# Performance work log

Hardware: AMD Instinct MI355X
Metric: run time of the kernel (lower is better)

## Reference

```python
import jax, jax.numpy as jnp
import numpy as np

NEG = jnp.float32(-1e10)

def setup_inputs() -> dict:
    key = jax.random.key(0)
    k1, k2, k3, k4 = jax.random.split(key, 4)
    B, Ns, Nr, D = 64, 512, 256, 1024
    return {
        "span_embeddings": jax.random.normal(k1, (B, Ns, D), dtype=jnp.float32),
        "image_embeddings": jax.random.normal(k2, (B, Nr, D), dtype=jnp.float32),
        "span_mask": jax.random.randint(k3, (B, Ns), 0, 2).astype(jnp.int32),
        "image_mask": jax.random.randint(k4, (B, Nr), 0, 2).astype(jnp.int32),
    }

def reference(span_embeddings, image_embeddings, span_mask, image_mask):
    # pair mask: (B, Ns, Nr) = image_mask[b, None, r] * span_mask[b, s, None]
    mask = (image_mask[:, None, :] * span_mask[:, :, None]).astype(span_embeddings.dtype)
    # QK^T with multiplicative mask, then custom zero->-1e10 masking
    att = jnp.einsum('bsd,brd->bsr', span_embeddings, image_embeddings) * mask
    att = jnp.where(att != 0, att, NEG)
    # spans attend over ROIs
    w_first = jax.nn.softmax(att, axis=-1) * mask
    att_first = jnp.einsum('bsr,brd->bsd', w_first, image_embeddings)
    score = jnp.mean(jnp.square(span_embeddings - att_first))
    # ROIs attend over spans (score_type='both')
    att_t = jnp.swapaxes(att, 1, 2)            # (B, Nr, Ns)
    w_second = jax.nn.softmax(att_t, axis=-1) * jnp.swapaxes(mask, 1, 2)
    att_second = jnp.einsum('brs,bsd->brd', w_second, span_embeddings)
    score = score + jnp.mean(jnp.square(image_embeddings - att_second))
    return score, att_first, att
```

## Files before the change

### kernel.cpp

```cpp
#include <hip/hip_runtime.h>
#include <hip/hip_bf16.h>
#include <math.h>

#define B_  64
#define NS  512
#define NR  256
#define DD  1024
#define NEGV (-1e10f)

typedef __attribute__((ext_vector_type(4))) float f32x4;
typedef __attribute__((ext_vector_type(8))) short bf16x8;

__device__ __forceinline__ unsigned short f2bf(float x) {
    unsigned u = __builtin_bit_cast(unsigned, x);
    unsigned r = u + 0x7FFFu + ((u >> 16) & 1u);
    return (unsigned short)(r >> 16);
}
__device__ __forceinline__ unsigned pk2(float x, float y) {
    unsigned r;
    asm("v_cvt_pk_bf16_f32 %0, %1, %2" : "=v"(r) : "v"(x), "v"(y));
    return r;
}
__device__ __forceinline__ void pk_hilo(float x, float y, unsigned& h, unsigned& l) {
    h = pk2(x, y);
    const float hx = __builtin_bit_cast(float, h << 16);
    const float hy = __builtin_bit_cast(float, h & 0xFFFF0000u);
    l = pk2(x - hx, y - hy);
}
__device__ __forceinline__ void gload16(const void* g, void* l) {
    __builtin_amdgcn_global_load_lds((const __attribute__((address_space(1))) void*)g,
                                     (__attribute__((address_space(3))) void*)l, 16, 0, 0);
}

__global__ __launch_bounds__(64) void zero_ws(double* ws) {
    if (threadIdx.x == 0) { ws[0] = 0.0; ws[1] = 0.0; }
}

__global__ __launch_bounds__(256) void att_mfma(
    const float* __restrict__ span, const float* __restrict__ image,
    const int* __restrict__ smask, const int* __restrict__ imask,
    float* __restrict__ att, float2* __restrict__ rowP, float2* __restrict__ colP,
    int doStats) {
    const int b  = blockIdx.z;
    const int s0 = blockIdx.y * 128;
    const int r0 = blockIdx.x * 128;
    __shared__ unsigned short Ah[128][40], Al[128][40], Bh[128][40], Bl[128][40];
    __shared__ float2 rowLDS[128][2];
    __shared__ float2 colLDS[128][2];
    const int tid  = threadIdx.x;
    const int lane = tid & 63;
    const int w    = tid >> 6;
    const int wso  = (w >> 1) * 64;
    const int wro  = (w & 1) * 64;
    const float* Sp = span  + ((size_t)b * NS + s0) * DD;
    const float* Im = image + ((size_t)b * NR + r0) * DD;

    f32x4 acc[4][4];
    #pragma unroll
    for (int i = 0; i < 4; ++i)
        #pragma unroll
        for (int j = 0; j < 4; ++j) acc[i][j] = (f32x4){0.f, 0.f, 0.f, 0.f};

    const int krel = (tid & 7) * 4;
    const int row0 = tid >> 3;
    const int fr   = lane & 15;
    const int fk   = (lane >> 4) * 8;

    float4 pa[4], pc[4];
    auto LOADK = [&](int k0) {
        #pragma unroll
        for (int p = 0; p < 4; ++p) {
            const int row = row0 + p * 32;
            pa[p] = *reinterpret_cast<const float4*>(Sp + (size_t)row * DD + k0 + krel);
            pc[p] = *reinterpret_cast<const float4*>(Im + (size_t)row * DD + k0 + krel);
        }
    };
    auto CONVW = [&]() {
        #pragma unroll
        for (int p = 0; p < 4; ++p) {
            const int row = row0 + p * 32;
            unsigned h0, l0, h1, l1;
            uint2 u;
            pk_hilo(pa[p].x, pa[p].y, h0, l0); pk_hilo(pa[p].z, pa[p].w, h1, l1);
            u.x = h0; u.y = h1; *reinterpret_cast<uint2*>(&Ah[row][krel]) = u;
            u.x = l0; u.y = l1; *reinterpret_cast<uint2*>(&Al[row][krel]) = u;
            pk_hilo(pc[p].x, pc[p].y, h0, l0); pk_hilo(pc[p].z, pc[p].w, h1, l1);
            u.x = h0; u.y = h1; *reinterpret_cast<uint2*>(&Bh[row][krel]) = u;
            u.x = l0; u.y = l1; *reinterpret_cast<uint2*>(&Bl[row][krel]) = u;
        }
    };
    auto FRAGMFMA = [&]() {
        bf16x8 ah[4], al[4], bh[4], bl[4];
        #pragma unroll
        for (int mf = 0; mf < 4; ++mf) {
            ah[mf] = *reinterpret_cast<const bf16x8*>(&Ah[wso + mf * 16 + fr][fk]);
            al[mf] = *reinterpret_cast<const bf16x8*>(&Al[wso + mf * 16 + fr][fk]);
            bh[mf] = *reinterpret_cast<const bf16x8*>(&Bh[wro + mf * 16 + fr][fk]);
            bl[mf] = *reinterpret_cast<const bf16x8*>(&Bl[wro + mf * 16 + fr][fk]);
        }
        #pragma unroll
        for (int mf = 0; mf < 4; ++mf)
            #pragma unroll
            for (int nf = 0; nf < 4; ++nf) {
                acc[mf][nf] = __builtin_amdgcn_mfma_f32_16x16x32_bf16(ah[mf], bh[nf], acc[mf][nf], 0, 0, 0);
                acc[mf][nf] = __builtin_amdgcn_mfma_f32_16x16x32_bf16(ah[mf], bl[nf], acc[mf][nf], 0, 0, 0);
                acc[mf][nf] = __builtin_amdgcn_mfma_f32_16x16x32_bf16(al[mf], bh[nf], acc[mf][nf], 0, 0, 0);
            }
    };

    LOADK(0); CONVW(); __syncthreads();
    for (int kt = 0; kt < 31; ++kt) {
        LOADK((kt + 1) * 32);
        FRAGMFMA();
        __syncthreads();
        CONVW();
        __syncthreads();
    }
    FRAGMFMA();

    const int fq = lane >> 4;
    float imvf[4];
    #pragma unroll
    for (int nf = 0; nf < 4; ++nf) imvf[nf] = (float)imask[b * NR + r0 + wro + nf * 16 + fr];
    float cmax[4] = {-3.4e38f, -3.4e38f, -3.4e38f, -3.4e38f};
    float smv[4][4];
    #pragma unroll
    for (int mf = 0; mf < 4; ++mf) {
        #pragma unroll
        for (int i = 0; i < 4; ++i) {
            const int s = s0 + wso + mf * 16 + fq * 4 + i;
            const float sv = (float)smask[b * NS + s];
            smv[mf][i] = sv;
            float* orow = att + ((size_t)b * NS + s) * NR + r0 + wro;
            float vj[4];
            #pragma unroll
            for (int nf = 0; nf < 4; ++nf) {
                float v = acc[mf][nf][i] * (sv * imvf[nf]);
                v = (v != 0.0f) ? v : NEGV;
                orow[nf * 16 + fr] = v;
                vj[nf] = v;
                cmax[nf] = fmaxf(cmax[nf], v);
            }
            if (doStats) {
                float rm = fmaxf(fmaxf(vj[0], vj[1]), fmaxf(vj[2], vj[3]));
                rm = fmaxf(rm, __shfl_xor(rm, 1));
                rm = fmaxf(rm, __shfl_xor(rm, 2));
                rm = fmaxf(rm, __shfl_xor(rm, 4));
                rm = fmaxf(rm, __shfl_xor(rm, 8));
                float rs = expf(vj[0] - rm) + expf(vj[1] - rm) + expf(vj[2] - rm) + expf(vj[3] - rm);
                rs += __shfl_xor(rs, 1);
                rs += __shfl_xor(rs, 2);
                rs += __shfl_xor(rs, 4);
                rs += __shfl_xor(rs, 8);
                if (fr == 0) rowLDS[wso + mf * 16 + fq * 4 + i][w & 1] = make_float2(rm, rs);
            }
        }
    }
    if (doStats) {
        #pragma unroll
        for (int nf = 0; nf < 4; ++nf) {
            cmax[nf] = fmaxf(cmax[nf], __shfl_xor(cmax[nf], 16));
            cmax[nf] = fmaxf(cmax[nf], __shfl_xor(cmax[nf], 32));
        }
        float csum[4] = {0.f, 0.f, 0.f, 0.f};
        #pragma unroll
        for (int mf = 0; mf < 4; ++mf)
            #pragma unroll
            for (int i = 0; i < 4; ++i)
                #pragma unroll
                for (int nf = 0; nf < 4; ++nf) {
                    float v = acc[mf][nf][i] * (smv[mf][i] * imvf[nf]);
                    v = (v != 0.0f) ? v : NEGV;
                    csum[nf] += expf(v - cmax[nf]);
                }
        #pragma unroll
        for (int nf = 0; nf < 4; ++nf) {
            csum[nf] += __shfl_xor(csum[nf], 16);
            csum[nf] += __shfl_xor(csum[nf], 32);
        }
        if (lane < 16) {
            #pragma unroll
            for (int nf = 0; nf < 4; ++nf)
                colLDS[wro + nf * 16 + lane][w >> 1] = make_float2(cmax[nf], csum[nf]);
        }
        __syncthreads();
        if (tid < 128) {
            const float2 q0 = rowLDS[tid][0], q1 = rowLDS[tid][1];
            const float m = fmaxf(q0.x, q1.x);
            const float ssum = q0.y * expf(q0.x - m) + q1.y * expf(q1.x - m);
            rowP[((size_t)b * NS + s0 + tid) * 2 + blockIdx.x] = make_float2(m, ssum);
        } else {
            const int c = tid - 128;
            const float2 q0 = colLDS[c][0], q1 = colLDS[c][1];
            const float m = fmaxf(q0.x, q1.x);
            const float ssum = q0.y * expf(q0.x - m) + q1.y * expf(q1.x - m);
            colP[((size_t)b * NR + r0 + c) * 4 + blockIdx.y] = make_float2(m, ssum);
        }
    }
}

__global__ __launch_bounds__(256) void combine_stats(
    const float2* __restrict__ rowP, const float2* __restrict__ colP,
    const int* __restrict__ smask, const int* __restrict__ imask,
    float* __restrict__ m1, float* __restrict__ f1,
    float* __restrict__ m2, float* __restrict__ f2) {
    const int idx = blockIdx.x * 256 + threadIdx.x;
    if (idx < B_ * NS) {
        const float2 p0 = rowP[(size_t)idx * 2 + 0];
        const float2 p1 = rowP[(size_t)idx * 2 + 1];
        const float m = fmaxf(p0.x, p1.x);
        const float s = p0.y * expf(p0.x - m) + p1.y * expf(p1.x - m);
        m1[idx] = m;
        f1[idx] = (float)smask[idx] / s;
    } else if (idx < B_ * NS + B_ * NR) {
        const int j = idx - B_ * NS;
        const float2 p0 = colP[(size_t)j * 4 + 0];
        const float2 p1 = colP[(size_t)j * 4 + 1];
        const float2 p2 = colP[(size_t)j * 4 + 2];
        const float2 p3 = colP[(size_t)j * 4 + 3];
        const float m = fmaxf(fmaxf(p0.x, p1.x), fmaxf(p2.x, p3.x));
        const float s = p0.y * expf(p0.x - m) + p1.y * expf(p1.x - m)
                      + p2.y * expf(p2.x - m) + p3.y * expf(p3.x - m);
        m2[j] = m;
        f2[j] = (float)imask[j] / s;
    }
}

__global__ __launch_bounds__(256) void transpose_swz(
    const float* __restrict__ src, unsigned short* __restrict__ dst, int N) {
    const int b = blockIdx.z, n0 = blockIdx.y * 32, d0 = blockIdx.x * 32;
    __shared__ unsigned short T[32][36];
    const int t = threadIdx.x;
    {
        const int n = t >> 3, dq = (t & 7) * 4;
        const float4 v = *reinterpret_cast<const float4*>(src + ((size_t)b * N + n0 + n) * DD + d0 + dq);
        T[dq + 0][n] = f2bf(v.x); T[dq + 1][n] = f2bf(v.y);
        T[dq + 2][n] = f2bf(v.z); T[dq + 3][n] = f2bf(v.w);
    }
    __syncthreads();
    {
        const int d = t >> 3, nq = (t & 7) * 4;
        const int dg = d0 + d;
        const int base = n0 + nq;
        const int pos = (base & 63) ^ ((dg & 7) << 3);
        const size_t idx = ((size_t)b * DD + dg) * N + (base & ~63) + pos;
        *reinterpret_cast<ushort4*>(dst + idx) = *reinterpret_cast<const ushort4*>(&T[d][nq]);
    }
}

__global__ __launch_bounds__(256) void build_w12(
    const float* __restrict__ att, const int* __restrict__ smask,
    const int* __restrict__ imask,
    const float* __restrict__ m1, const float* __restrict__ f1,
    const float* __restrict__ m2, const float* __restrict__ f2,
    unsigned short* __restrict__ w1g, unsigned short* __restrict__ w2g) {
    const int b = blockIdx.z, s0 = blockIdx.y * 64, r0 = blockIdx.x * 64;
    __shared__ unsigned short T[64][68];
    __shared__ float m2s[64], f2s[64], ims[64];
    const int tid = threadIdx.x;
    if (tid < 64) {
        m2s[tid] = m2[b * NR + r0 + tid];
        f2s[tid] = f2[b * NR + r0 + tid];
        ims[tid] = (float)imask[b * NR + r0 + tid];
    }
    __syncthreads();
    {
        const int srow = tid >> 2, rg = (tid & 3) * 16;
        const int s = s0 + srow;
        const float m1v = m1[b * NS + s], f1v = f1[b * NS + s];
        const float smv = (float)smask[b * NS + s];
        const float* arow = att + ((size_t)b * NS + s) * NR + r0;
        const int w1swz = (s & 7) << 3;
        unsigned short* w1row = w1g + ((size_t)b * NS + s) * NR + r0;
        #pragma unroll
        for (int g = 0; g < 4; ++g) {
            const int rr = rg + g * 4;
            const float4 a = *reinterpret_cast<const float4*>(arow + rr);
            const float e0 = expf(a.x - m1v) * f1v * ims[rr + 0];
            const float e1 = expf(a.y - m1v) * f1v * ims[rr + 1];
            const float e2 = expf(a.z - m1v) * f1v * ims[rr + 2];
            const float e3 = expf(a.w - m1v) * f1v * ims[rr + 3];
            uint2 u; u.x = pk2(e0, e1); u.y = pk2(e2, e3);
            *reinterpret_cast<uint2*>(w1row + (rr ^ w1swz)) = u;
            const float q0 = expf(a.x - m2s[rr + 0]) * f2s[rr + 0] * smv;
            const float q1 = expf(a.y - m2s[rr + 1]) * f2s[rr + 1] * smv;
            const float q2 = expf(a.z - m2s[rr + 2]) * f2s[rr + 2] * smv;
            const float q3 = expf(a.w - m2s[rr + 3]) * f2s[rr + 3] * smv;
            const unsigned t0 = pk2(q0, q1), t1 = pk2(q2, q3);
            T[rr + 0][srow] = (unsigned short)(t0 & 0xFFFF);
            T[rr + 1][srow] = (unsigned short)(t0 >> 16);
            T[rr + 2][srow] = (unsigned short)(t1 & 0xFFFF);
            T[rr + 3][srow] = (unsigned short)(t1 >> 16);
        }
    }
    __syncthreads();
    {
        const int rl = tid >> 2, sg = (tid & 3) * 16;
        const int w2swz = (rl & 7) << 3;
        unsigned short* w2row = w2g + ((size_t)b * NR + r0 + rl) * NS + s0;
        #pragma unroll
        for (int g = 0; g < 4; ++g) {
            const int ss = sg + g * 4;
            *reinterpret_cast<ushort4*>(w2row + (ss ^ w2swz)) =
                *reinterpret_cast<const ushort4*>(&T[rl][ss]);
        }
    }
}

template<int KTOT, int MT, bool WOUT, int WIDX>
__global__ __launch_bounds__(256) void gemm_apply(
    const unsigned short* __restrict__ Ag, const unsigned short* __restrict__ Btg,
    const float* __restrict__ ref, float* __restrict__ outp, double* __restrict__ wsum) {
    const int b = blockIdx.z, m0 = blockIdx.y * 64, d0 = blockIdx.x * 256;
    __shared__ unsigned short As[64 * 64];
    __shared__ unsigned short Bs[256 * 64];
    __shared__ float redsum[256];
    const int tid = threadIdx.x, lane = tid & 63, w = tid >> 6;
    const int fr = lane & 15, fq = lane >> 4;
    f32x4 acc[4][4];
    #pragma unroll
    for (int i = 0; i < 4; ++i)
        #pragma unroll
        for (int j = 0; j < 4; ++j) acc[i][j] = (f32x4){0.f, 0.f, 0.f, 0.f};

    const int srow = tid >> 3;
    const int scol = (tid & 7) * 16;
    for (int kc = 0; kc < KTOT / 64; ++kc) {
        const char* asrc = (const char*)(Ag + ((size_t)b * MT + m0) * KTOT) + kc * 128 + scol;
        #pragma unroll
        for (int c = 0; c < 2; ++c)
            gload16(asrc + (size_t)(c * 32 + srow) * (KTOT * 2), (char*)As + (c * 256 + tid) * 16);
        const char* bsrc = (const char*)(Btg + ((size_t)b * DD + d0) * KTOT) + kc * 128 + scol;
        #pragma unroll
        for (int c = 0; c < 8; ++c)
            gload16(bsrc + (size_t)(c * 32 + srow) * (KTOT * 2), (char*)Bs + (c * 256 + tid) * 16);
        __syncthreads();
        #pragma unroll
        for (int ks = 0; ks < 2; ++ks) {
            bf16x8 aF[4], bF[4];
            #pragma unroll
            for (int mf = 0; mf < 4; ++mf) {
                const int row = mf * 16 + fr;
                const int pos = (ks * 32 + fq * 8) ^ ((row & 7) << 3);
                aF[mf] = *reinterpret_cast<const bf16x8*>(&As[row * 64 + pos]);
            }
            #pragma unroll
            for (int nf = 0; nf < 4; ++nf) {
                const int row = w * 64 + nf * 16 + fr;
                const int pos = (ks * 32 + fq * 8) ^ ((row & 7) << 3);
                bF[nf] = *reinterpret_cast<const bf16x8*>(&Bs[row * 64 + pos]);
            }
            #pragma unroll
            for (int mf = 0; mf < 4; ++mf)
                #pragma unroll
                for (int nf = 0; nf < 4; ++nf)
                    acc[mf][nf] = __builtin_amdgcn_mfma_f32_16x16x32_bf16(aF[mf], bF[nf], acc[mf][nf], 0, 0, 0);
        }
        __syncthreads();
    }
    float sumsq = 0.0f;
    #pragma unroll
    for (int mf = 0; mf < 4; ++mf) {
        #pragma unroll
        for (int i = 0; i < 4; ++i) {
            const int row = m0 + mf * 16 + fq * 4 + i;
            const size_t base = ((size_t)b * MT + row) * DD + d0 + w * 64;
            #pragma unroll
            for (int nf = 0; nf < 4; ++nf) {
                const float v = acc[mf][nf][i];
                const float rv = ref[base + nf * 16 + fr];
                if constexpr (WOUT) outp[base + nf * 16 + fr] = v;
                const float dx = rv - v;
                sumsq += dx * dx;
            }
        }
    }
    redsum[tid] = sumsq; __syncthreads();
    for (int off = 128; off; off >>= 1) {
        if (tid < off) redsum[tid] += redsum[tid + off];
        __syncthreads();
    }
    if (tid == 0) atomicAdd(wsum + WIDX, (double)redsum[0]);
}

__global__ __launch_bounds__(256) void first_kernel(
    const float* __restrict__ span, const float* __restrict__ image,
    const int* __restrict__ smask, const int* __restrict__ imask,
    const float* __restrict__ att, float* __restrict__ att_first,
    double* __restrict__ ws) {
    const int b  = blockIdx.y;
    const int s0 = blockIdx.x * 32;
    __shared__ float wT[256][36];
    __shared__ float Is[32][132];
    __shared__ float red[256];
    const int tid  = threadIdx.x;
    const int lane = tid & 63, wave = tid >> 6;
    for (int i = 0; i < 8; ++i) {
        const int srel = wave * 8 + i;
        const int s    = s0 + srel;
        const float4 v = *reinterpret_cast<const float4*>(att + ((size_t)b * NS + s) * NR + lane * 4);
        float m = fmaxf(fmaxf(v.x, v.y), fmaxf(v.z, v.w));
        #pragma unroll
        for (int off = 32; off; off >>= 1) m = fmaxf(m, __shfl_xor(m, off));
        float4 e;
        e.x = expf(v.x - m); e.y = expf(v.y - m); e.z = expf(v.z - m); e.w = expf(v.w - m);
        float sum = e.x + e.y + e.z + e.w;
        #pragma unroll
        for (int off = 32; off; off >>= 1) sum += __shfl_xor(sum, off);
        const float fac = (float)smask[b * NS + s] / sum;
        const int4 im4 = *reinterpret_cast<const int4*>(imask + b * NR + lane * 4);
        wT[lane * 4 + 0][srel] = e.x * fac * (float)im4.x;
        wT[lane * 4 + 1][srel] = e.y * fac * (float)im4.y;
        wT[lane * 4 + 2][srel] = e.z * fac * (float)im4.z;
        wT[lane * 4 + 3][srel] = e.w * fac * (float)im4.w;
    }
    __syncthreads();
    float sumsq = 0.0f;
    const int txd = tid & 31;
    const int tys = tid >> 5;
    const float* Ib = image + (size_t)b * NR * DD;
    for (int dc = 0; dc < 8; ++dc) {
        const int d0 = dc * 128;
        float acc[4][4] = {};
        for (int rc = 0; rc < 8; ++rc) {
            const int r0 = rc * 32;
            {
                const int rr = tid >> 3;
                const int cb = tid & 7;
                const float* src = Ib + (size_t)(r0 + rr) * DD + d0;
                #pragma unroll
                for (int q = 0; q < 4; ++q)
                    *reinterpret_cast<float4*>(&Is[rr][(cb + 8 * q) * 4]) =
                        *reinterpret_cast<const float4*>(src + (cb + 8 * q) * 4);
            }
            __syncthreads();
            #pragma unroll 4
            for (int rr = 0; rr < 32; ++rr) {
                const float4 wv = *reinterpret_cast<const float4*>(&wT[r0 + rr][tys * 4]);
                const float4 iv = *reinterpret_cast<const float4*>(&Is[rr][txd * 4]);
                const float wvv[4] = {wv.x, wv.y, wv.z, wv.w};
                const float ivv[4] = {iv.x, iv.y, iv.z, iv.w};
                #pragma unroll
                for (int i = 0; i < 4; ++i)
                    #pragma unroll
                    for (int j = 0; j < 4; ++j)
                        acc[i][j] += wvv[i] * ivv[j];
            }
            __syncthreads();
        }
        #pragma unroll
        for (int i = 0; i < 4; ++i) {
            const int s = s0 + tys * 4 + i;
            const size_t base = ((size_t)b * NS + s) * DD + d0 + txd * 4;
            const float4 af = {acc[i][0], acc[i][1], acc[i][2], acc[i][3]};
            *reinterpret_cast<float4*>(att_first + base) = af;
            const float4 sp = *reinterpret_cast<const float4*>(span + base);
            float dx;
            dx = sp.x - af.x; sumsq += dx * dx;
            dx = sp.y - af.y; sumsq += dx * dx;
            dx = sp.z - af.z; sumsq += dx * dx;
            dx = sp.w - af.w; sumsq += dx * dx;
        }
    }
    red[tid] = sumsq; __syncthreads();
    for (int off = 128; off; off >>= 1) {
        if (tid < off) red[tid] += red[tid + off];
        __syncthreads();
    }
    if (tid == 0) atomicAdd(ws, (double)red[0]);
}

__global__ __launch_bounds__(256) void second_kernel(
    const float* __restrict__ span, const float* __restrict__ image,
    const int* __restrict__ smask, const int* __restrict__ imask,
    const float* __restrict__ att, double* __restrict__ ws) {
    const int b  = blockIdx.y;
    const int r0 = blockIdx.x * 32;
    __shared__ float w2s[32][36];
    __shared__ float Ss[32][132];
    __shared__ float mArr[32], fArr[32];
    __shared__ float redm[8][32];
    __shared__ float red[256];
    const int tid = threadIdx.x;
    const int rr = tid & 31, q = tid >> 5;
    const float* attb = att + (size_t)b * NS * NR + r0 + rr;
    float mloc = -3.4e38f;
    for (int t = 0; t < 64; ++t)
        mloc = fmaxf(mloc, attb[(size_t)(q * 64 + t) * NR]);
    redm[q][rr] = mloc;
    __syncthreads();
    if (tid < 32) {
        float m = redm[0][tid];
        #pragma unroll
        for (int qq = 1; qq < 8; ++qq) m = fmaxf(m, redm[qq][tid]);
        mArr[tid] = m;
    }
    __syncthreads();
    const float mcol = mArr[rr];
    float sloc = 0.0f;
    for (int t = 0; t < 64; ++t)
        sloc += expf(attb[(size_t)(q * 64 + t) * NR] - mcol);
    redm[q][rr] = sloc;
    __syncthreads();
    if (tid < 32) {
        float s = 0.0f;
        #pragma unroll
        for (int qq = 0; qq < 8; ++qq) s += redm[qq][tid];
        fArr[tid] = (float)imask[b * NR + r0 + tid] / s;
    }
    __syncthreads();
    float sumsq = 0.0f;
    const int txd = tid & 31;
    const int tyr = tid >> 5;
    const float* Sb = span + (size_t)b * NS * DD;
    for (int dc = 0; dc < 8; ++dc) {
        const int d0 = dc * 128;
        float acc[4][4] = {};
        for (int sc = 0; sc < 16; ++sc) {
            const int sb0 = sc * 32;
            {
                const int sr = tid >> 3;
                const int cb = tid & 7;
                const float* src = Sb + (size_t)(sb0 + sr) * DD + d0;
                #pragma unroll
                for (int qq = 0; qq < 4; ++qq)
                    *reinterpret_cast<float4*>(&Ss[sr][(cb + 8 * qq) * 4]) =
                        *reinterpret_cast<const float4*>(src + (cb + 8 * qq) * 4);
            }
            {
                const int ss = tid >> 3;
                const int rq = (tid & 7) * 4;
                const int s  = sb0 + ss;
                const float4 v = *reinterpret_cast<const float4*>(att + ((size_t)b * NS + s) * NR + r0 + rq);
                const float smv = (float)smask[b * NS + s];
                float4 wv;
                wv.x = expf(v.x - mArr[rq + 0]) * fArr[rq + 0] * smv;
                wv.y = expf(v.y - mArr[rq + 1]) * fArr[rq + 1] * smv;
                wv.z = expf(v.z - mArr[rq + 2]) * fArr[rq + 2] * smv;
                wv.w = expf(v.w - mArr[rq + 3]) * fArr[rq + 3] * smv;
                *reinterpret_cast<float4*>(&w2s[ss][rq]) = wv;
            }
            __syncthreads();
            #pragma unroll 4
            for (int ss = 0; ss < 32; ++ss) {
                const float4 wv = *reinterpret_cast<const float4*>(&w2s[ss][tyr * 4]);
                const float4 sv = *reinterpret_cast<const float4*>(&Ss[ss][txd * 4]);
                const float wvv[4] = {wv.x, wv.y, wv.z, wv.w};
                const float svv[4] = {sv.x, sv.y, sv.z, sv.w};
                #pragma unroll
                for (int i = 0; i < 4; ++i)
                    #pragma unroll
                    for (int j = 0; j < 4; ++j)
                        acc[i][j] += wvv[i] * svv[j];
            }
            __syncthreads();
        }
        #pragma unroll
        for (int i = 0; i < 4; ++i) {
            const int r = r0 + tyr * 4 + i;
            const float4 iv = *reinterpret_cast<const float4*>(image + ((size_t)b * NR + r) * DD + d0 + txd * 4);
            float dx;
            dx = iv.x - acc[i][0]; sumsq += dx * dx;
            dx = iv.y - acc[i][1]; sumsq += dx * dx;
            dx = iv.z - acc[i][2]; sumsq += dx * dx;
            dx = iv.w - acc[i][3]; sumsq += dx * dx;
        }
    }
    red[tid] = sumsq; __syncthreads();
    for (int off = 128; off; off >>= 1) {
        if (tid < off) red[tid] += red[tid + off];
        __syncthreads();
    }
    if (tid == 0) atomicAdd(ws + 1, (double)red[0]);
}

__global__ __launch_bounds__(64) void score_kernel(const double* __restrict__ ws, float* __restrict__ out) {
    if (threadIdx.x == 0) {
        out[0] = (float)(ws[0] / (double)((size_t)B_ * NS * DD) +
                         ws[1] / (double)((size_t)B_ * NR * DD));
    }
}

extern "C" void kernel_launch(void* const* d_in, const int* in_sizes, int n_in,
                              void* d_out, int out_size, void* d_ws, size_t ws_size,
                              hipStream_t stream) {
    const float* span  = (const float*)d_in[0];
    const float* image = (const float*)d_in[1];
    const int*   smask = (const int*)d_in[2];
    const int*   imask = (const int*)d_in[3];
    float* out       = (float*)d_out;
    float* att_first = out + 1;
    float* att       = out + 1 + (size_t)B_ * NS * DD;

    char* base = (char*)d_ws;
    double* wsum = (double*)base;
    float* m1 = (float*)(base + 512);
    float* f1 = m1 + (size_t)B_ * NS;
    float* m2 = f1 + (size_t)B_ * NS;
    float* f2 = m2 + (size_t)B_ * NR;
    float2* rowP = (float2*)(f2 + (size_t)B_ * NR);
    float2* colP = rowP + (size_t)B_ * NS * 2;
    char* X0 = (char*)(colP + (size_t)B_ * NR * 4);
    unsigned short* imgT = (unsigned short*)X0;
    unsigned short* w1g  = (unsigned short*)(X0 + (size_t)B_ * DD * NR * 2);
    unsigned short* spT  = (unsigned short*)X0;
    unsigned short* w2g  = (unsigned short*)(X0 + (size_t)B_ * DD * NS * 2);
    const size_t NEED = (size_t)(X0 - base) + (size_t)B_ * DD * NS * 2 + (size_t)B_ * NS * NR * 2;
    const int wsok = (ws_size >= NEED) ? 1 : 0;

    zero_ws<<<dim3(1), dim3(64), 0, stream>>>(wsum);
    att_mfma<<<dim3(NR / 128, NS / 128, B_), dim3(256), 0, stream>>>(
        span, image, smask, imask, att, rowP, colP, wsok);

    if (wsok) {
        combine_stats<<<dim3((B_ * NS + B_ * NR) / 256), dim3(256), 0, stream>>>(
            rowP, colP, smask, imask, m1, f1, m2, f2);
        transpose_swz<<<dim3(DD / 32, NR / 32, B_), dim3(256), 0, stream>>>(image, imgT, NR);
        build_w12<<<dim3(NR / 64, NS / 64, B_), dim3(256), 0, stream>>>(
            att, smask, imask, m1, f1, m2, f2, w1g, w2g);
        gemm_apply<NR, NS, true, 0><<<dim3(DD / 256, NS / 64, B_), dim3(256), 0, stream>>>(
            w1g, imgT, span, att_first, wsum);
        transpose_swz<<<dim3(DD / 32, NS / 32, B_), dim3(256), 0, stream>>>(span, spT, NS);
        gemm_apply<NS, NR, false, 1><<<dim3(DD / 256, NR / 64, B_), dim3(256), 0, stream>>>(
            w2g, spT, image, nullptr, wsum);
    } else {
        first_kernel<<<dim3(NS / 32, B_), dim3(256), 0, stream>>>(span, image, smask, imask, att, att_first, wsum);
        second_kernel<<<dim3(NR / 32, B_), dim3(256), 0, stream>>>(span, image, smask, imask, att, wsum);
    }
    score_kernel<<<dim3(1), dim3(64), 0, stream>>>(wsum, out);
}
```

Baseline: 306.1 us.

## Move softmax sum computation from GEMM epilogue into weight build and apply normalization late

The QK^T kernel now records only row and column maxima, dropping the exp-sum passes and the online max/sum merging. build_w12 computes the exponentials once, accumulates row and column sums with atomics, and writes unnormalized bf16 weights. The mask/sum normalization factor is applied per output row in the gemm_apply epilogue. The QK^T main loop also loses its register prefetch double-buffering and becomes a simple load-convert-sync loop, which may expose more global load latency. Changes: atomics contention, fast __expf, column sums taken from bf16-rounded values.

New measurement: 310.5 us. No clear change (+1.5%).

```diff
diff --git a/kernel.cpp b/kernel.cpp
--- a/kernel.cpp
+++ b/kernel.cpp
@@ -16,6 +16,10 @@
     unsigned r = u + 0x7FFFu + ((u >> 16) & 1u);
     return (unsigned short)(r >> 16);
 }
+__device__ __forceinline__ float bf2f(unsigned short h) {
+    unsigned u = ((unsigned)h) << 16;
+    return __builtin_bit_cast(float, u);
+}
 __device__ __forceinline__ unsigned pk2(float x, float y) {
     unsigned r;
     asm("v_cvt_pk_bf16_f32 %0, %1, %2" : "=v"(r) : "v"(x), "v"(y));
@@ -39,14 +43,12 @@
 __global__ __launch_bounds__(256) void att_mfma(
     const float* __restrict__ span, const float* __restrict__ image,
     const int* __restrict__ smask, const int* __restrict__ imask,
-    float* __restrict__ att, float2* __restrict__ rowP, float2* __restrict__ colP,
+    float* __restrict__ att, float* __restrict__ rowP, float* __restrict__ colP,
     int doStats) {
     const int b  = blockIdx.z;
     const int s0 = blockIdx.y * 128;
     const int r0 = blockIdx.x * 128;
     __shared__ unsigned short Ah[128][40], Al[128][40], Bh[128][40], Bl[128][40];
-    __shared__ float2 rowLDS[128][2];
-    __shared__ float2 colLDS[128][2];
     const int tid  = threadIdx.x;
     const int lane = tid & 63;
     const int w    = tid >> 6;
@@ -66,30 +68,22 @@
     const int fr   = lane & 15;
     const int fk   = (lane >> 4) * 8;
 
-    float4 pa[4], pc[4];
-    auto LOADK = [&](int k0) {
+    for (int k0 = 0; k0 < DD; k0 += 32) {
         #pragma unroll
         for (int p = 0; p < 4; ++p) {
             const int row = row0 + p * 32;
-            pa[p] = *reinterpret_cast<const float4*>(Sp + (size_t)row * DD + k0 + krel);
-            pc[p] = *reinterpret_cast<const float4*>(Im + (size_t)row * DD + k0 + krel);
-        }
-    };
-    auto CONVW = [&]() {
-        #pragma unroll
-        for (int p = 0; p < 4; ++p) {
-            const int row = row0 + p * 32;
+            const float4 a = *reinterpret_cast<const float4*>(Sp + (size_t)row * DD + k0 + krel);
+            const float4 c = *reinterpret_cast<const float4*>(Im + (size_t)row * DD + k0 + krel);
             unsigned h0, l0, h1, l1;
             uint2 u;
-            pk_hilo(pa[p].x, pa[p].y, h0, l0); pk_hilo(pa[p].z, pa[p].w, h1, l1);
+            pk_hilo(a.x, a.y, h0, l0); pk_hilo(a.z, a.w, h1, l1);
             u.x = h0; u.y = h1; *reinterpret_cast<uint2*>(&Ah[row][krel]) = u;
             u.x = l0; u.y = l1; *reinterpret_cast<uint2*>(&Al[row][krel]) = u;
-            pk_hilo(pc[p].x, pc[p].y, h0, l0); pk_hilo(pc[p].z, pc[p].w, h1, l1);
+            pk_hilo(c.x, c.y, h0, l0); pk_hilo(c.z, c.w, h1, l1);
             u.x = h0; u.y = h1; *reinterpret_cast<uint2*>(&Bh[row][krel]) = u;
             u.x = l0; u.y = l1; *reinterpret_cast<uint2*>(&Bl[row][krel]) = u;
         }
-    };
-    auto FRAGMFMA = [&]() {
+        __syncthreads();
         bf16x8 ah[4], al[4], bh[4], bl[4];
         #pragma unroll
         for (int mf = 0; mf < 4; ++mf) {
@@ -106,36 +100,27 @@
                 acc[mf][nf] = __builtin_amdgcn_mfma_f32_16x16x32_bf16(ah[mf], bl[nf], acc[mf][nf], 0, 0, 0);
                 acc[mf][nf] = __builtin_amdgcn_mfma_f32_16x16x32_bf16(al[mf], bh[nf], acc[mf][nf], 0, 0, 0);
             }
-    };
-
-    LOADK(0); CONVW(); __syncthreads();
-    for (int kt = 0; kt < 31; ++kt) {
-        LOADK((kt + 1) * 32);
-        FRAGMFMA();
-        __syncthreads();
-        CONVW();
-        __syncthreads();
-    }
-    FRAGMFMA();
-
+        __syncthreads();
+    }
+
+    float* rowLDS = reinterpret_cast<float*>(&Ah[0][0]);
+    float* colLDS = rowLDS + 256;
     const int fq = lane >> 4;
-    float imvf[4];
+    int imv[4];
     #pragma unroll
-    for (int nf = 0; nf < 4; ++nf) imvf[nf] = (float)imask[b * NR + r0 + wro + nf * 16 + fr];
+    for (int nf = 0; nf < 4; ++nf) imv[nf] = imask[b * NR + r0 + wro + nf * 16 + fr];
     float cmax[4] = {-3.4e38f, -3.4e38f, -3.4e38f, -3.4e38f};
-    float smv[4][4];
     #pragma unroll
     for (int mf = 0; mf < 4; ++mf) {
         #pragma unroll
         for (int i = 0; i < 4; ++i) {
             const int s = s0 + wso + mf * 16 + fq * 4 + i;
-            const float sv = (float)smask[b * NS + s];
-            smv[mf][i] = sv;
+            const int sm = smask[b * NS + s];
             float* orow = att + ((size_t)b * NS + s) * NR + r0 + wro;
             float vj[4];
             #pragma unroll
             for (int nf = 0; nf < 4; ++nf) {
-                float v = acc[mf][nf][i] * (sv * imvf[nf]);
+                float v = acc[mf][nf][i] * (float)(sm * imv[nf]);
                 v = (v != 0.0f) ? v : NEGV;
                 orow[nf * 16 + fr] = v;
                 vj[nf] = v;
@@ -147,12 +132,7 @@
                 rm = fmaxf(rm, __shfl_xor(rm, 2));
                 rm = fmaxf(rm, __shfl_xor(rm, 4));
                 rm = fmaxf(rm, __shfl_xor(rm, 8));
-                float rs = expf(vj[0] - rm) + expf(vj[1] - rm) + expf(vj[2] - rm) + expf(vj[3] - rm);
-                rs += __shfl_xor(rs, 1);
-                rs += __shfl_xor(rs, 2);
-                rs += __shfl_xor(rs, 4);
-                rs += __shfl_xor(rs, 8);
-                if (fr == 0) rowLDS[wso + mf * 16 + fq * 4 + i][w & 1] = make_float2(rm, rs);
+                if (fr == 0) rowLDS[(wso + mf * 16 + fq * 4 + i) * 2 + (w & 1)] = rm;
             }
         }
     }
@@ -162,67 +142,36 @@
             cmax[nf] = fmaxf(cmax[nf], __shfl_xor(cmax[nf], 16));
             cmax[nf] = fmaxf(cmax[nf], __shfl_xor(cmax[nf], 32));
         }
-        float csum[4] = {0.f, 0.f, 0.f, 0.f};
-        #pragma unroll
-        for (int mf = 0; mf < 4; ++mf)
-            #pragma unroll
-            for (int i = 0; i < 4; ++i)
-                #pragma unroll
-                for (int nf = 0; nf < 4; ++nf) {
-                    float v = acc[mf][nf][i] * (smv[mf][i] * imvf[nf]);
-                    v = (v != 0.0f) ? v : NEGV;
-                    csum[nf] += expf(v - cmax[nf]);
-                }
-        #pragma unroll
-        for (int nf = 0; nf < 4; ++nf) {
-            csum[nf] += __shfl_xor(csum[nf], 16);
-            csum[nf] += __shfl_xor(csum[nf], 32);
-        }
         if (lane < 16) {
             #pragma unroll
             for (int nf = 0; nf < 4; ++nf)
-                colLDS[wro + nf * 16 + lane][w >> 1] = make_float2(cmax[nf], csum[nf]);
+                colLDS[(wro + nf * 16 + lane) * 2 + (w >> 1)] = cmax[nf];
         }
         __syncthreads();
         if (tid < 128) {
-            const float2 q0 = rowLDS[tid][0], q1 = rowLDS[tid][1];
-            const float m = fmaxf(q0.x, q1.x);
-            const float ssum = q0.y * expf(q0.x - m) + q1.y * expf(q1.x - m);
-            rowP[((size_t)b * NS + s0 + tid) * 2 + blockIdx.x] = make_float2(m, ssum);
+            rowP[((size_t)b * NS + s0 + tid) * 2 + blockIdx.x] =
+                fmaxf(rowLDS[tid * 2 + 0], rowLDS[tid * 2 + 1]);
         } else {
             const int c = tid - 128;
-            const float2 q0 = colLDS[c][0], q1 = colLDS[c][1];
-            const float m = fmaxf(q0.x, q1.x);
-            const float ssum = q0.y * expf(q0.x - m) + q1.y * expf(q1.x - m);
-            colP[((size_t)b * NR + r0 + c) * 4 + blockIdx.y] = make_float2(m, ssum);
-        }
-    }
-}
-
-__global__ __launch_bounds__(256) void combine_stats(
-    const float2* __restrict__ rowP, const float2* __restrict__ colP,
-    const int* __restrict__ smask, const int* __restrict__ imask,
-    float* __restrict__ m1, float* __restrict__ f1,
-    float* __restrict__ m2, float* __restrict__ f2) {
+            colP[((size_t)b * NR + r0 + c) * 4 + blockIdx.y] =
+                fmaxf(colLDS[c * 2 + 0], colLDS[c * 2 + 1]);
+        }
+    }
+}
+
+__global__ __launch_bounds__(256) void combine_max(
+    const float* __restrict__ rowP, const float* __restrict__ colP,
+    float* __restrict__ m1, float* __restrict__ m2,
+    float* __restrict__ rowsum1, float* __restrict__ colsum2) {
     const int idx = blockIdx.x * 256 + threadIdx.x;
     if (idx < B_ * NS) {
-        const float2 p0 = rowP[(size_t)idx * 2 + 0];
-        const float2 p1 = rowP[(size_t)idx * 2 + 1];
-        const float m = fmaxf(p0.x, p1.x);
-        const float s = p0.y * expf(p0.x - m) + p1.y * expf(p1.x - m);
-        m1[idx] = m;
-        f1[idx] = (float)smask[idx] / s;
+        m1[idx] = fmaxf(rowP[(size_t)idx * 2 + 0], rowP[(size_t)idx * 2 + 1]);
+        rowsum1[idx] = 0.0f;
     } else if (idx < B_ * NS + B_ * NR) {
         const int j = idx - B_ * NS;
-        const float2 p0 = colP[(size_t)j * 4 + 0];
-        const float2 p1 = colP[(size_t)j * 4 + 1];
-        const float2 p2 = colP[(size_t)j * 4 + 2];
-        const float2 p3 = colP[(size_t)j * 4 + 3];
-        const float m = fmaxf(fmaxf(p0.x, p1.x), fmaxf(p2.x, p3.x));
-        const float s = p0.y * expf(p0.x - m) + p1.y * expf(p1.x - m)
-                      + p2.y * expf(p2.x - m) + p3.y * expf(p3.x - m);
-        m2[j] = m;
-        f2[j] = (float)imask[j] / s;
+        m2[j] = fmaxf(fmaxf(colP[(size_t)j * 4 + 0], colP[(size_t)j * 4 + 1]),
+                      fmaxf(colP[(size_t)j * 4 + 2], colP[(size_t)j * 4 + 3]));
+        colsum2[j] = 0.0f;
     }
 }
 
@@ -251,66 +200,84 @@
 __global__ __launch_bounds__(256) void build_w12(
     const float* __restrict__ att, const int* __restrict__ smask,
     const int* __restrict__ imask,
-    const float* __restrict__ m1, const float* __restrict__ f1,
-    const float* __restrict__ m2, const float* __restrict__ f2,
-    unsigned short* __restrict__ w1g, unsigned short* __restrict__ w2g) {
+    const float* __restrict__ m1, const float* __restrict__ m2,
+    unsigned short* __restrict__ w1g, unsigned short* __restrict__ w2g,
+    float* __restrict__ rowsum1, float* __restrict__ colsum2) {
     const int b = blockIdx.z, s0 = blockIdx.y * 64, r0 = blockIdx.x * 64;
     __shared__ unsigned short T[64][68];
-    __shared__ float m2s[64], f2s[64], ims[64];
+    __shared__ float m2s[64], ims[64], sms[64];
     const int tid = threadIdx.x;
     if (tid < 64) {
         m2s[tid] = m2[b * NR + r0 + tid];
-        f2s[tid] = f2[b * NR + r0 + tid];
         ims[tid] = (float)imask[b * NR + r0 + tid];
+        sms[tid] = (float)smask[b * NS + s0 + tid];
     }
     __syncthreads();
     {
         const int srow = tid >> 2, rg = (tid & 3) * 16;
         const int s = s0 + srow;
-        const float m1v = m1[b * NS + s], f1v = f1[b * NS + s];
-        const float smv = (float)smask[b * NS + s];
+        const float m1v = m1[b * NS + s];
         const float* arow = att + ((size_t)b * NS + s) * NR + r0;
         const int w1swz = (s & 7) << 3;
         unsigned short* w1row = w1g + ((size_t)b * NS + s) * NR + r0;
+        float rsum = 0.0f;
         #pragma unroll
         for (int g = 0; g < 4; ++g) {
             const int rr = rg + g * 4;
             const float4 a = *reinterpret_cast<const float4*>(arow + rr);
-            const float e0 = expf(a.x - m1v) * f1v * ims[rr + 0];
-            const float e1 = expf(a.y - m1v) * f1v * ims[rr + 1];
-            const float e2 = expf(a.z - m1v) * f1v * ims[rr + 2];
-            const float e3 = expf(a.w - m1v) * f1v * ims[rr + 3];
-            uint2 u; u.x = pk2(e0, e1); u.y = pk2(e2, e3);
+            const float e0 = __expf(a.x - m1v);
+            const float e1 = __expf(a.y - m1v);
+            const float e2 = __expf(a.z - m1v);
+            const float e3 = __expf(a.w - m1v);
+            rsum += (e0 + e1) + (e2 + e3);
+            uint2 u;
+            u.x = pk2(e0 * ims[rr + 0], e1 * ims[rr + 1]);
+            u.y = pk2(e2 * ims[rr + 2], e3 * ims[rr + 3]);
             *reinterpret_cast<uint2*>(w1row + (rr ^ w1swz)) = u;
-            const float q0 = expf(a.x - m2s[rr + 0]) * f2s[rr + 0] * smv;
-            const float q1 = expf(a.y - m2s[rr + 1]) * f2s[rr + 1] * smv;
-            const float q2 = expf(a.z - m2s[rr + 2]) * f2s[rr + 2] * smv;
-            const float q3 = expf(a.w - m2s[rr + 3]) * f2s[rr + 3] * smv;
+            const float q0 = __expf(a.x - m2s[rr + 0]);
+            const float q1 = __expf(a.y - m2s[rr + 1]);
+            const float q2 = __expf(a.z - m2s[rr + 2]);
+            const float q3 = __expf(a.w - m2s[rr + 3]);
             const unsigned t0 = pk2(q0, q1), t1 = pk2(q2, q3);
             T[rr + 0][srow] = (unsigned short)(t0 & 0xFFFF);
             T[rr + 1][srow] = (unsigned short)(t0 >> 16);
             T[rr + 2][srow] = (unsigned short)(t1 & 0xFFFF);
             T[rr + 3][srow] = (unsigned short)(t1 >> 16);
         }
+        rsum += __shfl_xor(rsum, 1);
+        rsum += __shfl_xor(rsum, 2);
+        if ((tid & 3) == 0) atomicAdd(&rowsum1[b * NS + s], rsum);
     }
     __syncthreads();
     {
         const int rl = tid >> 2, sg = (tid & 3) * 16;
         const int w2swz = (rl & 7) << 3;
         unsigned short* w2row = w2g + ((size_t)b * NR + r0 + rl) * NS + s0;
+        float csum = 0.0f;
         #pragma unroll
         for (int g = 0; g < 4; ++g) {
             const int ss = sg + g * 4;
-            *reinterpret_cast<ushort4*>(w2row + (ss ^ w2swz)) =
-                *reinterpret_cast<const ushort4*>(&T[rl][ss]);
-        }
+            const ushort4 t = *reinterpret_cast<const ushort4*>(&T[rl][ss]);
+            csum += (bf2f(t.x) + bf2f(t.y)) + (bf2f(t.z) + bf2f(t.w));
+            ushort4 o;
+            o.x = (sms[ss + 0] != 0.0f) ? t.x : (unsigned short)0;
+            o.y = (sms[ss + 1] != 0.0f) ? t.y : (unsigned short)0;
+            o.z = (sms[ss + 2] != 0.0f) ? t.z : (unsigned short)0;
+            o.w = (sms[ss + 3] != 0.0f) ? t.w : (unsigned short)0;
+            *reinterpret_cast<ushort4*>(w2row + (ss ^ w2swz)) = o;
+        }
+        csum += __shfl_xor(csum, 1);
+        csum += __shfl_xor(csum, 2);
+        if ((tid & 3) == 0) atomicAdd(&colsum2[b * NR + r0 + rl], csum);
     }
 }
 
 template<int KTOT, int MT, bool WOUT, int WIDX>
 __global__ __launch_bounds__(256) void gemm_apply(
     const unsigned short* __restrict__ Ag, const unsigned short* __restrict__ Btg,
-    const float* __restrict__ ref, float* __restrict__ outp, double* __restrict__ wsum) {
+    const float* __restrict__ ref, float* __restrict__ outp,
+    const int* __restrict__ rmask, const float* __restrict__ rsum,
+    double* __restrict__ wsum) {
     const int b = blockIdx.z, m0 = blockIdx.y * 64, d0 = blockIdx.x * 256;
     __shared__ unsigned short As[64 * 64];
     __shared__ unsigned short Bs[256 * 64];
@@ -364,10 +331,12 @@
         #pragma unroll
         for (int i = 0; i < 4; ++i) {
             const int row = m0 + mf * 16 + fq * 4 + i;
-            const size_t base = ((size_t)b * MT + row) * DD + d0 + w * 64;
+            const size_t gidx = (size_t)b * MT + row;
+            const float fac = (float)rmask[gidx] / rsum[gidx];
+            const size_t base = gidx * DD + d0 + w * 64;
             #pragma unroll
             for (int nf = 0; nf < 4; ++nf) {
-                const float v = acc[mf][nf][i];
+                const float v = acc[mf][nf][i] * fac;
                 const float rv = ref[base + nf * 16 + fr];
                 if constexpr (WOUT) outp[base + nf * 16 + fr] = v;
                 const float dx = rv - v;
@@ -594,12 +563,12 @@
 
     char* base = (char*)d_ws;
     double* wsum = (double*)base;
-    float* m1 = (float*)(base + 512);
-    float* f1 = m1 + (size_t)B_ * NS;
-    float* m2 = f1 + (size_t)B_ * NS;
-    float* f2 = m2 + (size_t)B_ * NR;
-    float2* rowP = (float2*)(f2 + (size_t)B_ * NR);
-    float2* colP = rowP + (size_t)B_ * NS * 2;
+    float* m1      = (float*)(base + 512);
+    float* m2      = m1 + (size_t)B_ * NS;
+    float* rowsum1 = m2 + (size_t)B_ * NR;
+    float* colsum2 = rowsum1 + (size_t)B_ * NS;
+    float* rowP    = colsum2 + (size_t)B_ * NR;
+    float* colP    = rowP + (size_t)B_ * NS * 2;
     char* X0 = (char*)(colP + (size_t)B_ * NR * 4);
     unsigned short* imgT = (unsigned short*)X0;
     unsigned short* w1g  = (unsigned short*)(X0 + (size_t)B_ * DD * NR * 2);
@@ -613,16 +582,16 @@
         span, image, smask, imask, att, rowP, colP, wsok);
 
     if (wsok) {
-        combine_stats<<<dim3((B_ * NS + B_ * NR) / 256), dim3(256), 0, stream>>>(
-            rowP, colP, smask, imask, m1, f1, m2, f2);
+        combine_max<<<dim3((B_ * NS + B_ * NR) / 256), dim3(256), 0, stream>>>(
+            rowP, colP, m1, m2, rowsum1, colsum2);
         transpose_swz<<<dim3(DD / 32, NR / 32, B_), dim3(256), 0, stream>>>(image, imgT, NR);
         build_w12<<<dim3(NR / 64, NS / 64, B_), dim3(256), 0, stream>>>(
-            att, smask, imask, m1, f1, m2, f2, w1g, w2g);
+            att, smask, imask, m1, m2, w1g, w2g, rowsum1, colsum2);
         gemm_apply<NR, NS, true, 0><<<dim3(DD / 256, NS / 64, B_), dim3(256), 0, stream>>>(
-            w1g, imgT, span, att_first, wsum);
+            w1g, imgT, span, att_first, smask, rowsum1, wsum);
         transpose_swz<<<dim3(DD / 32, NS / 32, B_), dim3(256), 0, stream>>>(span, spT, NS);
         gemm_apply<NS, NR, false, 1><<<dim3(DD / 256, NR / 64, B_), dim3(256), 0, stream>>>(
-            w2g, spT, image, nullptr, wsum);
+            w2g, spT, image, nullptr, imask, colsum2, wsum);
     } else {
         first_kernel<<<dim3(NS / 32, B_), dim3(256), 0, stream>>>(span, image, smask, imask, att, att_first, wsum);
         second_kernel<<<dim3(NR / 32, B_), dim3(256), 0, stream>>>(span, image, smask, imask, att, wsum);
```
